# Kernel optimization log

Measured on AMD Instinct MI355X. Metric: run time of the kernel, lower is better.

The kernel has to match this reference:

```python
import jax, jax.numpy as jnp
import numpy as np

B, T, D, H = 4, 2048, 768, 12
DH = D // H
SCALE = DH ** 0.5


def setup_inputs() -> dict:
    key = jax.random.key(0)
    k1, k2, k3, k4, k5, k6 = jax.random.split(key, 6)
    h = jax.random.normal(k1, (B, T, D), dtype=jnp.float32)
    key_padding_mask = jax.random.bernoulli(k2, 0.1, (B, T))
    s = 1.0 / np.sqrt(D)
    Wq = jax.random.normal(k3, (D, D), dtype=jnp.float32) * s
    Wk = jax.random.normal(k4, (D, D), dtype=jnp.float32) * s
    Wv = jax.random.normal(k5, (D, D), dtype=jnp.float32) * s
    Wo = jax.random.normal(k6, (D, D), dtype=jnp.float32) * s
    return {"h": h, "key_padding_mask": key_padding_mask,
            "Wq": Wq, "Wk": Wk, "Wv": Wv, "Wo": Wo}


def _split_heads(x):
    Bb, Tt, _ = x.shape
    return x.reshape(Bb, Tt, H, DH).transpose(0, 2, 1, 3)  # [B,H,T,Dh]


def reference(h, key_padding_mask, Wq, Wk, Wv, Wo):
    # torch nn.Linear (no bias): y = x @ W.T
    Q = _split_heads(h @ Wq.T)
    K = _split_heads(h @ Wk.T)
    V = _split_heads(h @ Wv.T)
    scores = jnp.einsum('bhqd,bhkd->bhqk', Q, K) / SCALE
    k_pad = key_padding_mask[:, None, None, :]  # mask padded keys
    q_pad = key_padding_mask[:, None, :, None]  # padded query rows
    scores = jnp.where(k_pad, jnp.float32(-1e9), scores)
    scores = jnp.where(q_pad, jnp.float32(0.0), scores)
    attn = jax.nn.softmax(scores, axis=-1)  # stable softmax (same math)
    attn = jnp.where(q_pad, jnp.float32(0.0), attn)
    out = jnp.einsum('bhqk,bhkd->bhqd', attn, V)  # [B,H,T,Dh]
    out = out.transpose(0, 2, 1, 3).reshape(B, T, D)
    return out @ Wo.T
```

## Files before the change

kernel.cpp:

```cpp
#include <hip/hip_runtime.h>
#include <stdint.h>

typedef __bf16 bf16x8 __attribute__((ext_vector_type(8)));
typedef float  f32x4  __attribute__((ext_vector_type(4)));
typedef float  f32x16 __attribute__((ext_vector_type(16)));
typedef unsigned short u16x4 __attribute__((ext_vector_type(4)));

#define MFMA16(a,b,c) __builtin_amdgcn_mfma_f32_16x16x32_bf16((a),(b),(c),0,0,0)
#define MFMA32(a,b,c) __builtin_amdgcn_mfma_f32_32x32x16_bf16((a),(b),(c),0,0,0)

constexpr int Bc  = 4;
constexpr int Tc  = 2048;
constexpr int Dc  = 768;
constexpr int Hc  = 12;
constexpr int NTOK = Bc * Tc;
constexpr int QKV_N = 3 * Dc;
constexpr int QK_LD = 2 * Dc;

static __device__ __forceinline__ unsigned short f2bf(float f){
  unsigned u = __float_as_uint(f);
  u += 0x7fffu + ((u >> 16) & 1u);
  return (unsigned short)(u >> 16);
}

static __device__ __forceinline__ float exp2a(float x){
  float r; asm("v_exp_f32 %0, %1" : "=v"(r) : "v"(x)); return r;
}

static __device__ __forceinline__ float max3f(float a, float b, float c){
  float r; asm("v_max3_f32 %0, %1, %2, %3" : "=v"(r) : "v"(a), "v"(b), "v"(c)); return r;
}

static __device__ __forceinline__ unsigned cvtpk_bf16(float lo, float hi){
  unsigned r; asm("v_cvt_pk_bf16_f32 %0, %1, %2" : "=v"(r) : "v"(lo), "v"(hi)); return r;
}

static __device__ __forceinline__ void gload_lds16(const void* g, void* l){
  __builtin_amdgcn_global_load_lds((__attribute__((address_space(1))) void*)g,
                                   (__attribute__((address_space(3))) void*)l,
                                   16, 0, 0);
}

__global__ void cvt_bf16(const float* __restrict__ src, unsigned short* __restrict__ dst,
                         int n4, float scale){
  int i = blockIdx.x * blockDim.x + threadIdx.x;
  if (i >= n4) return;
  float4 v = reinterpret_cast<const float4*>(src)[i];
  ushort4 o;
  o.x = f2bf(v.x * scale); o.y = f2bf(v.y * scale);
  o.z = f2bf(v.z * scale); o.w = f2bf(v.w * scale);
  reinterpret_cast<ushort4*>(dst)[i] = o;
}

__global__ void cvt_w4(const float* __restrict__ Wq, const float* __restrict__ Wk,
                       const float* __restrict__ Wv, const float* __restrict__ Wo,
                       unsigned short* __restrict__ Wqkv, unsigned short* __restrict__ Wob,
                       int n4, float qscale){
  const int y = blockIdx.y;
  const float* src = (y==0) ? Wq : (y==1) ? Wk : (y==2) ? Wv : Wo;
  unsigned short* dst = (y==3) ? Wob : Wqkv + (size_t)y * n4 * 4;
  const float scale = (y==0) ? qscale : 1.0f;
  int i = blockIdx.x * blockDim.x + threadIdx.x;
  if (i >= n4) return;
  float4 v = reinterpret_cast<const float4*>(src)[i];
  ushort4 o;
  o.x = f2bf(v.x * scale); o.y = f2bf(v.y * scale);
  o.z = f2bf(v.z * scale); o.w = f2bf(v.w * scale);
  reinterpret_cast<ushort4*>(dst)[i] = o;
}

__global__ void expand_mask(const unsigned* __restrict__ raw, int* __restrict__ out, int n){
  __shared__ int sInt, sFlt;
  int t = threadIdx.x;
  if (t == 0){ sInt = 1; sFlt = 1; }
  __syncthreads();
  int okI = 1, okF = 1;
  for (int i = t; i < n/4; i += blockDim.x){
    unsigned u = raw[i];
    okI &= (u <= 1u);
    okF &= (u == 0u || u == 0x3f800000u);
  }
  if (!okI) atomicAnd(&sInt, 0);
  if (!okF) atomicAnd(&sFlt, 0);
  __syncthreads();
  if (sInt || sFlt){
    for (int i = t; i < n; i += blockDim.x) out[i] = (raw[i] != 0u);
  } else {
    const unsigned char* rb = (const unsigned char*)raw;
    for (int i = t; i < n; i += blockDim.x) out[i] = (rb[i] != 0);
  }
}

__global__ __launch_bounds__(256) void gemm_qkv(const unsigned short* __restrict__ A,
                                                const unsigned short* __restrict__ Bm,
                                                unsigned short* __restrict__ QKt,
                                                unsigned short* __restrict__ VtG,
                                                int M, int N, int K){
  __shared__ unsigned short As[128*32];
  __shared__ unsigned short Bs[128*32];
  const int t = threadIdx.x;
  const int w = t >> 6, l = t & 63;
  const int wr = w >> 1, wc = w & 1;
  const int br = blockIdx.y * 128, bc = blockIdx.x * 128;

  f32x4 acc[4][4];
  const f32x4 fz = {0.f,0.f,0.f,0.f};
  #pragma unroll
  for (int m=0;m<4;m++)
    #pragma unroll
    for (int n=0;n<4;n++) acc[m][n] = fz;

  const int lrow = l >> 2;
  const int lk   = (l & 3) * 8;
  const int fr   = l & 15;
  const int fk   = (l >> 4) * 8;

  for (int k0 = 0; k0 < K; k0 += 32){
    #pragma unroll
    for (int it = 0; it < 2; ++it){
      const int rb = it*64 + w*16;
      gload_lds16(A  + (size_t)(br + rb + lrow)*K + k0 + lk, &As[rb*32]);
      gload_lds16(Bm + (size_t)(bc + rb + lrow)*K + k0 + lk, &Bs[rb*32]);
    }
    __syncthreads();
    bf16x8 a[4], b[4];
    #pragma unroll
    for (int m=0;m<4;m++)
      a[m] = *reinterpret_cast<const bf16x8*>(&As[(wr*64 + m*16 + fr)*32 + fk]);
    #pragma unroll
    for (int n=0;n<4;n++)
      b[n] = *reinterpret_cast<const bf16x8*>(&Bs[(wc*64 + n*16 + fr)*32 + fk]);
    #pragma unroll
    for (int m=0;m<4;m++)
      #pragma unroll
      for (int n=0;n<4;n++)
        acc[m][n] = MFMA16(a[m], b[n], acc[m][n]);
    __syncthreads();
  }

  const int orow0 = br + wr*64 + (l >> 4)*4;
  const int ocol0 = bc + wc*64 + (l & 15);
  if (bc >= QK_LD){
    #pragma unroll
    for (int m=0;m<4;m++){
      const int orow = orow0 + m*16;
      const int bb = orow >> 11, tok = orow & 2047;
      #pragma unroll
      for (int n=0;n<4;n++){
        const int cc = ocol0 + n*16 - QK_LD;
        const int hh = cc >> 6, dd = cc & 63;
        ushort4 o;
        o.x = f2bf(acc[m][n][0]); o.y = f2bf(acc[m][n][1]);
        o.z = f2bf(acc[m][n][2]); o.w = f2bf(acc[m][n][3]);
        *reinterpret_cast<ushort4*>(
            &VtG[((size_t)((bb*Hc + hh)*64 + dd))*Tc + tok]) = o;
      }
    }
  } else {
    #pragma unroll
    for (int m=0;m<4;m++)
      #pragma unroll
      for (int n=0;n<4;n++)
        #pragma unroll
        for (int r=0;r<4;r++)
          QKt[(size_t)(orow0 + m*16 + r) * QK_LD + (ocol0 + n*16)] =
              f2bf(acc[m][n][r]);
  }
}

__global__ __launch_bounds__(256) void gemm_bt64(const unsigned short* __restrict__ A,
                                                 const unsigned short* __restrict__ Bm,
                                                 float* __restrict__ C,
                                                 int M, int N, int K){
  __shared__ unsigned short As[64*32];
  __shared__ unsigned short Bs[128*32];
  const int t = threadIdx.x;
  const int w = t >> 6, l = t & 63;
  const int wr = w >> 1, wc = w & 1;
  const int br = blockIdx.y * 64, bc = blockIdx.x * 128;

  f32x4 acc[2][4];
  const f32x4 fz = {0.f,0.f,0.f,0.f};
  #pragma unroll
  for (int m=0;m<2;m++)
    #pragma unroll
    for (int n=0;n<4;n++) acc[m][n] = fz;

  const int lrow = l >> 2;
  const int lk   = (l & 3) * 8;
  const int fr   = l & 15;
  const int fk   = (l >> 4) * 8;

  for (int k0 = 0; k0 < K; k0 += 32){
    gload_lds16(A + (size_t)(br + w*16 + lrow)*K + k0 + lk, &As[(w*16)*32]);
    #pragma unroll
    for (int it = 0; it < 2; ++it){
      const int rb = it*64 + w*16;
      gload_lds16(Bm + (size_t)(bc + rb + lrow)*K + k0 + lk, &Bs[rb*32]);
    }
    __syncthreads();
    bf16x8 a[2], b[4];
    #pragma unroll
    for (int m=0;m<2;m++)
      a[m] = *reinterpret_cast<const bf16x8*>(&As[(wr*32 + m*16 + fr)*32 + fk]);
    #pragma unroll
    for (int n=0;n<4;n++)
      b[n] = *reinterpret_cast<const bf16x8*>(&Bs[(wc*64 + n*16 + fr)*32 + fk]);
    #pragma unroll
    for (int m=0;m<2;m++)
      #pragma unroll
      for (int n=0;n<4;n++)
        acc[m][n] = MFMA16(a[m], b[n], acc[m][n]);
    __syncthreads();
  }

  const int orow0 = br + wr*32 + (l >> 4)*4;
  const int ocol0 = bc + wc*64 + (l & 15);
  #pragma unroll
  for (int m=0;m<2;m++)
    #pragma unroll
    for (int n=0;n<4;n++)
      #pragma unroll
      for (int r=0;r<4;r++)
        C[(size_t)(orow0 + m*16 + r) * N + (ocol0 + n*16)] = acc[m][n][r];
}

__global__ __launch_bounds__(256, 3) void attn(const unsigned short* __restrict__ QKt,
                                               const unsigned short* __restrict__ VtG,
                                               const int* __restrict__ mask,
                                               unsigned short* __restrict__ AO){
  __shared__ unsigned short Ks[2][64*64];
  __shared__ unsigned short Vs[2][64*64];
  __shared__ float Ms[2][64];

  const int t = threadIdx.x, w = t >> 6, l = t & 63;
  const int lin = blockIdx.y * gridDim.x + blockIdx.x;
  const int swz = (lin & 7) * 96 + (lin >> 3);
  const int qt  = swz & 15;
  const int bh  = swz >> 4;
  const int b  = bh / Hc, h = bh - b * Hc;
  const int lq = l & 31, hi = l >> 5;
  const int q0w = qt * 128 + w * 32;

  const size_t tokbase = (size_t)b * Tc;
  const unsigned short* Qp = QKt + (tokbase + q0w) * (size_t)QK_LD + h*64;
  const unsigned short* Kbase = QKt + tokbase * (size_t)QK_LD + h*64 + 768;
  const unsigned short* VtB = VtG + (size_t)(bh*64) * Tc;
  const int* bm = mask + b * Tc;

  bf16x8 qa[4];
  #pragma unroll
  for (int s=0; s<4; s++)
    qa[s] = *reinterpret_cast<const bf16x8*>(
        Qp + (size_t)lq*QK_LD + s*16 + hi*8);

  unsigned bits = 0;
  if (w == 0){
    #pragma unroll
    for (int cc = 0; cc < 32; ++cc)
      bits |= (unsigned)(bm[cc*64 + l] != 0) << cc;
  }

  f32x16 accO[2];
  #pragma unroll
  for (int dg=0; dg<2; dg++)
    #pragma unroll
    for (int r=0; r<16; r++) accO[dg][r] = 0.f;
  float mrow = -1e30f, lsum = 0.f;

  const int srow = l >> 3, scol = (l & 7) ^ (l >> 3);
  auto stage = [&](int c){
    const int key0 = c * 64, buf = c & 1;
    #pragma unroll
    for (int i=0; i<2; i++){
      const int rb = w*16 + i*8;
      gload_lds16(Kbase + (size_t)(key0 + rb + srow)*QK_LD + scol*8,
                  &Ks[buf][rb*64]);
    }
    #pragma unroll
    for (int i=0; i<2; i++){
      const int rb = (w*2 + i)*8;
      gload_lds16(VtB + (size_t)(rb + srow)*Tc + key0 + scol*8,
                  &Vs[buf][rb*64]);
    }
  };

  stage(0);
  if (w == 0) Ms[0][l] = (bits & 1u) ? -1e9f : 0.f;
  asm volatile("s_waitcnt vmcnt(0) lgkmcnt(0)" ::: "memory");
  __builtin_amdgcn_s_barrier();
  asm volatile("" ::: "memory");

  #pragma unroll 2
  for (int c = 0; c < 32; ++c){
    const int cb = c & 1;

    f32x16 S[2];
    __builtin_amdgcn_s_setprio(1);
    #pragma unroll
    for (int g=0; g<2; g++){
      union { f32x4 q[4]; f32x16 v; } mi;
      #pragma unroll
      for (int m=0; m<4; m++)
        mi.q[m] = *reinterpret_cast<const f32x4*>(&Ms[cb][g*32 + m*8 + hi*4]);
      S[g] = mi.v;
      #pragma unroll
      for (int s=0; s<4; s++){
        const int row = g*32 + lq;
        bf16x8 kf = *reinterpret_cast<const bf16x8*>(
            &Ks[cb][row*64 + (((2*s + hi) ^ (row&7))*8)]);
        S[g] = MFMA32(kf, qa[s], S[g]);
      }
    }
    __builtin_amdgcn_s_setprio(0);

    if (c + 1 < 32) stage(c + 1);

    unsigned pk[2][2][4];
    {
      float m0 = max3f(S[0][0],  S[0][1],  S[0][2]);
      float m1 = max3f(S[0][3],  S[0][4],  S[0][5]);
      float m2 = max3f(S[0][6],  S[0][7],  S[0][8]);
      float m3 = max3f(S[0][9],  S[0][10], S[0][11]);
      float m4 = max3f(S[0][12], S[0][13], S[0][14]);
      float m5 = max3f(S[0][15], S[1][0],  S[1][1]);
      float m6 = max3f(S[1][2],  S[1][3],  S[1][4]);
      float m7 = max3f(S[1][5],  S[1][6],  S[1][7]);
      float m8 = max3f(S[1][8],  S[1][9],  S[1][10]);
      float m9 = max3f(S[1][11], S[1][12], S[1][13]);
      float ma = fmaxf(S[1][14], S[1][15]);
      float cm = max3f(max3f(m0,m1,m2), max3f(m3,m4,m5),
                       max3f(max3f(m6,m7,m8), m9, ma));
      cm = fmaxf(cm, __shfl_xor(cm, 32));
      if (!__all(cm <= mrow + 8.0f)){
        const float nm = fmaxf(mrow, cm);
        const float sc = exp2a(mrow - nm);
        lsum *= sc;
        #pragma unroll
        for (int dg=0; dg<2; dg++)
          #pragma unroll
          for (int r=0; r<16; r++) accO[dg][r] *= sc;
        mrow = nm;
      }
      float ps = 0.f;
      #pragma unroll
      for (int g=0; g<2; g++){
        float p[16];
        #pragma unroll
        for (int r=0; r<16; r++) p[r] = exp2a(S[g][r] - mrow);
        float t0 = (p[0]+p[1]) + (p[2]+p[3]);
        float t1 = (p[4]+p[5]) + (p[6]+p[7]);
        float t2 = (p[8]+p[9]) + (p[10]+p[11]);
        float t3 = (p[12]+p[13]) + (p[14]+p[15]);
        ps += (t0+t1) + (t2+t3);
        #pragma unroll
        for (int ss=0; ss<2; ss++)
          #pragma unroll
          for (int j2=0; j2<4; j2++)
            pk[g][ss][j2] = cvtpk_bf16(p[ss*8 + 2*j2], p[ss*8 + 2*j2 + 1]);
      }
      ps += __shfl_xor(ps, 32);
      lsum += ps;
    }

    __builtin_amdgcn_s_setprio(1);
    #pragma unroll
    for (int g=0; g<2; g++){
      #pragma unroll
      for (int ss=0; ss<2; ss++){
        union { unsigned u[4]; bf16x8 v; } pb;
        pb.u[0] = pk[g][ss][0]; pb.u[1] = pk[g][ss][1];
        pb.u[2] = pk[g][ss][2]; pb.u[3] = pk[g][ss][3];
        const int u0 = 4*g + 2*ss;
        #pragma unroll
        for (int dg=0; dg<2; dg++){
          const int d = dg*32 + lq;
          union { u16x4 h[2]; bf16x8 v; } va;
          va.h[0] = *reinterpret_cast<const u16x4*>(
              &Vs[cb][d*64 + ((u0     ^ (d&7))*8) + hi*4]);
          va.h[1] = *reinterpret_cast<const u16x4*>(
              &Vs[cb][d*64 + (((u0+1) ^ (d&7))*8) + hi*4]);
          accO[dg] = MFMA32(va.v, pb.v, accO[dg]);
        }
      }
    }
    __builtin_amdgcn_s_setprio(0);

    if (w == 0 && c + 1 < 32)
      Ms[cb^1][l] = ((bits >> (c+1)) & 1u) ? -1e9f : 0.f;

    if (c < 31){
      asm volatile("s_waitcnt vmcnt(0) lgkmcnt(0)" ::: "memory");
      __builtin_amdgcn_s_barrier();
      asm volatile("" ::: "memory");
    }
  }

  {
    const int qrow = q0w + lq;
    const int qm = bm[qrow];
    const float inv = (qm || lsum <= 0.f) ? 0.f : 1.f / lsum;
    #pragma unroll
    for (int dg=0; dg<2; dg++)
      #pragma unroll
      for (int m=0; m<4; m++){
        ushort4 o;
        o.x = f2bf(accO[dg][4*m+0] * inv);
        o.y = f2bf(accO[dg][4*m+1] * inv);
        o.z = f2bf(accO[dg][4*m+2] * inv);
        o.w = f2bf(accO[dg][4*m+3] * inv);
        *reinterpret_cast<ushort4*>(
            &AO[(tokbase + qrow) * (size_t)Dc + h*64 + dg*32 + m*8 + hi*4]) = o;
      }
  }
}

extern "C" void kernel_launch(void* const* d_in, const int* in_sizes, int n_in,
                              void* d_out, int out_size, void* d_ws, size_t ws_size,
                              hipStream_t stream){
  const float* h    = (const float*)d_in[0];
  const unsigned* m = (const unsigned*)d_in[1];
  const float* Wq   = (const float*)d_in[2];
  const float* Wk   = (const float*)d_in[3];
  const float* Wv   = (const float*)d_in[4];
  const float* Wo   = (const float*)d_in[5];
  float* out        = (float*)d_out;

  unsigned short* hb   = (unsigned short*)d_ws;
  unsigned short* Wqkv = hb   + (size_t)NTOK * Dc;
  unsigned short* Wob  = Wqkv + (size_t)QKV_N * Dc;
  unsigned short* QKt  = Wob  + (size_t)Dc * Dc;
  unsigned short* VtG  = QKt  + (size_t)NTOK * QK_LD;
  unsigned short* AO   = VtG  + (size_t)NTOK * Dc;
  int* mexp            = (int*)(AO + (size_t)NTOK * Dc);

  const size_t need = ((size_t)NTOK*Dc + (size_t)QKV_N*Dc + (size_t)Dc*Dc +
                       (size_t)NTOK*QK_LD + (size_t)NTOK*Dc + (size_t)NTOK*Dc) * 2
                      + (size_t)NTOK*4;
  if (ws_size < need) return;

  const int W2 = Dc * Dc;
  cvt_bf16<<<(NTOK*Dc/4 + 255)/256, 256, 0, stream>>>(h, hb, NTOK*Dc/4, 1.0f);
  cvt_w4<<<dim3((W2/4 + 255)/256, 4), 256, 0, stream>>>(
      Wq, Wk, Wv, Wo, Wqkv, Wob, W2/4, 0.125f*1.44269504f);
  expand_mask<<<1, 256, 0, stream>>>(m, mexp, NTOK);

  gemm_qkv<<<dim3(QKV_N/128, NTOK/128), 256, 0, stream>>>(
      hb, Wqkv, QKt, VtG, NTOK, QKV_N, Dc);

  attn<<<dim3(16, Bc*Hc), 256, 0, stream>>>(QKt, VtG, mexp, AO);

  gemm_bt64<<<dim3(Dc/128, NTOK/64), 256, 0, stream>>>(
      AO, Wob, out, NTOK, Dc, Dc);
}
```

Measured before the change: 174.6 us.

## Deepen QKV GEMM K-tile with XOR-swizzled LDS, remap blocks, fuse conversion kernels

The QKV projection GEMM now stages 64-wide K slices instead of 32, which halves the number of barrier pairs per tile. It uses an XOR swizzle on LDS columns to avoid bank conflicts when fragments are read. Both GEMMs remap block indices so that consecutive workgroups are spread across the grid, aiming for better L2 reuse and channel spread. The separate activation and weight bf16 conversion kernels are merged into one launch to cut launch overhead, at the cost of a divide per thread and doubled LDS use in the QKV GEMM.

```diff
diff --git a/kernel.cpp b/kernel.cpp
--- a/kernel.cpp
+++ b/kernel.cpp
@@ -16,6 +16,8 @@
 constexpr int NTOK = Bc * Tc;
 constexpr int QKV_N = 3 * Dc;
 constexpr int QK_LD = 2 * Dc;
+constexpr int H4 = NTOK * Dc / 4;
+constexpr int W4 = Dc * Dc / 4;
 
 static __device__ __forceinline__ unsigned short f2bf(float f){
   unsigned u = __float_as_uint(f);
@@ -41,32 +43,30 @@
                                    16, 0, 0);
 }
 
-__global__ void cvt_bf16(const float* __restrict__ src, unsigned short* __restrict__ dst,
-                         int n4, float scale){
-  int i = blockIdx.x * blockDim.x + threadIdx.x;
-  if (i >= n4) return;
-  float4 v = reinterpret_cast<const float4*>(src)[i];
+__global__ void prep(const float* __restrict__ h,  const float* __restrict__ Wq,
+                     const float* __restrict__ Wk, const float* __restrict__ Wv,
+                     const float* __restrict__ Wo,
+                     unsigned short* __restrict__ hb,
+                     unsigned short* __restrict__ Wqkv,
+                     unsigned short* __restrict__ Wob, float qscale){
+  const int idx = blockIdx.x * blockDim.x + threadIdx.x;
+  const float* src; ushort4* dst; float sc = 1.0f; int r;
+  if (idx < H4){
+    src = h; dst = reinterpret_cast<ushort4*>(hb); r = idx;
+  } else {
+    const int j = idx - H4;
+    const int y = j / W4;
+    r = j - y * W4;
+    if (y == 0){ src = Wq; sc = qscale; } else if (y == 1){ src = Wk; }
+    else if (y == 2){ src = Wv; } else { src = Wo; }
+    dst = (y == 3) ? reinterpret_cast<ushort4*>(Wob)
+                   : reinterpret_cast<ushort4*>(Wqkv) + (size_t)y * W4;
+  }
+  float4 v = reinterpret_cast<const float4*>(src)[r];
   ushort4 o;
-  o.x = f2bf(v.x * scale); o.y = f2bf(v.y * scale);
-  o.z = f2bf(v.z * scale); o.w = f2bf(v.w * scale);
-  reinterpret_cast<ushort4*>(dst)[i] = o;
-}
-
-__global__ void cvt_w4(const float* __restrict__ Wq, const float* __restrict__ Wk,
-                       const float* __restrict__ Wv, const float* __restrict__ Wo,
-                       unsigned short* __restrict__ Wqkv, unsigned short* __restrict__ Wob,
-                       int n4, float qscale){
-  const int y = blockIdx.y;
-  const float* src = (y==0) ? Wq : (y==1) ? Wk : (y==2) ? Wv : Wo;
-  unsigned short* dst = (y==3) ? Wob : Wqkv + (size_t)y * n4 * 4;
-  const float scale = (y==0) ? qscale : 1.0f;
-  int i = blockIdx.x * blockDim.x + threadIdx.x;
-  if (i >= n4) return;
-  float4 v = reinterpret_cast<const float4*>(src)[i];
-  ushort4 o;
-  o.x = f2bf(v.x * scale); o.y = f2bf(v.y * scale);
-  o.z = f2bf(v.z * scale); o.w = f2bf(v.w * scale);
-  reinterpret_cast<ushort4*>(dst)[i] = o;
+  o.x = f2bf(v.x * sc); o.y = f2bf(v.y * sc);
+  o.z = f2bf(v.z * sc); o.w = f2bf(v.w * sc);
+  dst[r] = o;
 }
 
 __global__ void expand_mask(const unsigned* __restrict__ raw, int* __restrict__ out, int n){
@@ -96,12 +96,15 @@
                                                 unsigned short* __restrict__ QKt,
                                                 unsigned short* __restrict__ VtG,
                                                 int M, int N, int K){
-  __shared__ unsigned short As[128*32];
-  __shared__ unsigned short Bs[128*32];
+  __shared__ unsigned short As[128*64];
+  __shared__ unsigned short Bs[128*64];
   const int t = threadIdx.x;
   const int w = t >> 6, l = t & 63;
   const int wr = w >> 1, wc = w & 1;
-  const int br = blockIdx.y * 128, bc = blockIdx.x * 128;
+  const int lin = blockIdx.y * gridDim.x + blockIdx.x;
+  const int swz = (lin & 7) * 144 + (lin >> 3);
+  const int bxs = swz % 18, bys = swz / 18;
+  const int br = bys * 128, bc = bxs * 128;
 
   f32x4 acc[4][4];
   const f32x4 fz = {0.f,0.f,0.f,0.f};
@@ -110,31 +113,42 @@
     #pragma unroll
     for (int n=0;n<4;n++) acc[m][n] = fz;
 
-  const int lrow = l >> 2;
-  const int lk   = (l & 3) * 8;
-  const int fr   = l & 15;
-  const int fk   = (l >> 4) * 8;
-
-  for (int k0 = 0; k0 < K; k0 += 32){
-    #pragma unroll
-    for (int it = 0; it < 2; ++it){
-      const int rb = it*64 + w*16;
-      gload_lds16(A  + (size_t)(br + rb + lrow)*K + k0 + lk, &As[rb*32]);
-      gload_lds16(Bm + (size_t)(bc + rb + lrow)*K + k0 + lk, &Bs[rb*32]);
+  const int srow = l >> 3;
+  const int scol = (l & 7) ^ srow;
+  const int fr = l & 15;
+  const int fu = l >> 4;
+
+  for (int k0 = 0; k0 < K; k0 += 64){
+    #pragma unroll
+    for (int i = 0; i < 4; ++i){
+      const int rb = w*32 + i*8;
+      gload_lds16(A  + (size_t)(br + rb + srow)*K + k0 + scol*8, &As[rb*64]);
+      gload_lds16(Bm + (size_t)(bc + rb + srow)*K + k0 + scol*8, &Bs[rb*64]);
     }
     __syncthreads();
-    bf16x8 a[4], b[4];
-    #pragma unroll
-    for (int m=0;m<4;m++)
-      a[m] = *reinterpret_cast<const bf16x8*>(&As[(wr*64 + m*16 + fr)*32 + fk]);
-    #pragma unroll
-    for (int n=0;n<4;n++)
-      b[n] = *reinterpret_cast<const bf16x8*>(&Bs[(wc*64 + n*16 + fr)*32 + fk]);
-    #pragma unroll
-    for (int m=0;m<4;m++)
-      #pragma unroll
-      for (int n=0;n<4;n++)
-        acc[m][n] = MFMA16(a[m], b[n], acc[m][n]);
+    bf16x8 a[2][4], b[2][4];
+    #pragma unroll
+    for (int ks=0; ks<2; ks++){
+      #pragma unroll
+      for (int m=0;m<4;m++){
+        const int row = wr*64 + m*16 + fr;
+        a[ks][m] = *reinterpret_cast<const bf16x8*>(
+            &As[row*64 + (((ks*4+fu) ^ (row&7))*8)]);
+      }
+      #pragma unroll
+      for (int n=0;n<4;n++){
+        const int row = wc*64 + n*16 + fr;
+        b[ks][n] = *reinterpret_cast<const bf16x8*>(
+            &Bs[row*64 + (((ks*4+fu) ^ (row&7))*8)]);
+      }
+    }
+    #pragma unroll
+    for (int ks=0; ks<2; ks++)
+      #pragma unroll
+      for (int m=0;m<4;m++)
+        #pragma unroll
+        for (int n=0;n<4;n++)
+          acc[m][n] = MFMA16(a[ks][m], b[ks][n], acc[m][n]);
     __syncthreads();
   }
 
@@ -177,7 +191,10 @@
   const int t = threadIdx.x;
   const int w = t >> 6, l = t & 63;
   const int wr = w >> 1, wc = w & 1;
-  const int br = blockIdx.y * 64, bc = blockIdx.x * 128;
+  const int lin = blockIdx.y * gridDim.x + blockIdx.x;
+  const int swz = (lin & 7) * 96 + (lin >> 3);
+  const int bxs = swz % 6, bys = swz / 6;
+  const int br = bys * 64, bc = bxs * 128;
 
   f32x4 acc[2][4];
   const f32x4 fz = {0.f,0.f,0.f,0.f};
@@ -439,10 +456,8 @@
                       + (size_t)NTOK*4;
   if (ws_size < need) return;
 
-  const int W2 = Dc * Dc;
-  cvt_bf16<<<(NTOK*Dc/4 + 255)/256, 256, 0, stream>>>(h, hb, NTOK*Dc/4, 1.0f);
-  cvt_w4<<<dim3((W2/4 + 255)/256, 4), 256, 0, stream>>>(
-      Wq, Wk, Wv, Wo, Wqkv, Wob, W2/4, 0.125f*1.44269504f);
+  prep<<<(H4 + 4*W4 + 255)/256, 256, 0, stream>>>(
+      h, Wq, Wk, Wv, Wo, hb, Wqkv, Wob, 0.125f*1.44269504f);
   expand_mask<<<1, 256, 0, stream>>>(m, mexp, NTOK);
 
   gemm_qkv<<<dim3(QKV_N/128, NTOK/128), 256, 0, stream>>>(
```

Result: faster. 170.2 us (-2.5%).
